# Performance work log

Measured on AMD Instinct MI355X. Metric: run time of the kernel, lower is better.

The kernel has to match this reference:

```python
import jax, jax.numpy as jnp
import numpy as np

EPS = 1e-5  # torch LayerNorm default

def ln(x, g, b):
    mu = jnp.mean(x, axis=-1, keepdims=True)
    var = jnp.mean((x - mu) ** 2, axis=-1, keepdims=True)
    return (x - mu) * jax.lax.rsqrt(var + EPS) * g + b

B, S, E, A = 131072, 199, 3, 32
D_IN = S + 1  # state_dim + 1 (time feature)

def setup_inputs() -> dict:
    key = jax.random.key(0)
    ks = iter(jax.random.split(key, 32))
    def w(shape, fan_in):
        lim = 1.0 / np.sqrt(fan_in)
        return jax.random.uniform(next(ks), shape, jnp.float32, -lim, lim)
    inp = {
        "state": jax.random.normal(next(ks), (B, S), jnp.float32),
        "time_delta": jax.random.uniform(next(ks), (B,), jnp.float32),
        # trunk: Linear(200,256)+LN, Linear(256,256)+LN, Linear(256,128)+LN
        "W1": w((D_IN, 256), D_IN), "b1": w((256,), D_IN),
        "g1": jnp.ones((256,), jnp.float32), "be1": jnp.zeros((256,), jnp.float32),
        "W2": w((256, 256), 256), "b2": w((256,), 256),
        "g2": jnp.ones((256,), jnp.float32), "be2": jnp.zeros((256,), jnp.float32),
        "W3": w((256, 128), 256), "b3": w((128,), 256),
        "g3": jnp.ones((128,), jnp.float32), "be3": jnp.zeros((128,), jnp.float32),
        # value stream
        "Wv1": w((128, 64), 128), "bv1": w((64,), 128),
        "gv": jnp.ones((64,), jnp.float32), "bev": jnp.zeros((64,), jnp.float32),
        "Wv2": w((64, 1), 64), "bv2": w((1,), 64),
        # E stacked advantage streams (all heads share action dim A)
        "Wa1": w((E, 128, 64), 128), "ba1": w((E, 64), 128),
        "ga": jnp.ones((E, 64), jnp.float32), "bea": jnp.zeros((E, 64), jnp.float32),
        "Wa2": w((E, 64, A), 64), "ba2": w((E, A), 64),
        "event_type": jax.random.randint(next(ks), (B,), 0, E),
    }
    return inp

def reference(state, time_delta,
              W1, b1, g1, be1, W2, b2, g2, be2, W3, b3, g3, be3,
              Wv1, bv1, gv, bev, Wv2, bv2,
              Wa1, ba1, ga, bea, Wa2, ba2, event_type):
    td = time_delta[:, None]                       # [B,1]
    x = jnp.concatenate([state, td], axis=1)       # [B,200]
    h = jax.nn.relu(ln(x @ W1 + b1, g1, be1))      # [B,256]
    h = jax.nn.relu(ln(h @ W2 + b2, g2, be2))      # [B,256]
    f = jax.nn.relu(ln(h @ W3 + b3, g3, be3))      # [B,128]
    v = jax.nn.relu(ln(f @ Wv1 + bv1, gv, bev)) @ Wv2 + bv2  # [B,1]
    # compute all E advantage heads, then per-sample select by event_type
    h1 = jnp.einsum('bd,edh->ebh', f, Wa1) + ba1[:, None, :]           # [E,B,64]
    h1 = jax.nn.relu(ln(h1, ga[:, None, :], bea[:, None, :]))
    adv_all = jnp.einsum('ebh,eha->eba', h1, Wa2) + ba2[:, None, :]    # [E,B,A]
    adv = jnp.take_along_axis(adv_all, event_type[None, :, None], axis=0)[0]  # [B,A]
    return v + (adv - adv.mean(axis=1, keepdims=True))
```

## Files before the change

kernel.cpp:

```cpp
#include <hip/hip_runtime.h>
#include <hip/hip_bf16.h>
#include <stdint.h>

#define DEV __device__ __forceinline__

typedef __attribute__((ext_vector_type(8))) short short8;
typedef __attribute__((ext_vector_type(4))) float floatx4;

constexpr int TM  = 64;
constexpr int NB  = 131072;
constexpr int AST = 264;

constexpr int OFF_W1 = 0;
constexpr int OFF_W2 = 57344;
constexpr int OFF_W3 = 122880;
constexpr int OFF_WH = 155648;
constexpr int OFF_WA2= 188416;
constexpr int NWQ    = 194560;

constexpr int C_B1=0, C_G1=256, C_BE1=512, C_B2=768, C_G2=1024, C_BE2=1280,
  C_B3=1536, C_G3=1664, C_BE3=1792, C_BV1=1920, C_GV=1984, C_BEV=2048,
  C_WV2=2112, C_BV2=2176, C_BA1=2180, C_GA=2372, C_BEA=2564, C_BA2=2756;
constexpr int NCONST=2852;

struct Ptrs {
  const float *state,*td,*W1,*b1,*g1,*be1,*W2,*b2,*g2,*be2,*W3,*b3,*g3,*be3,
    *Wv1,*bv1,*gv,*bev,*Wv2,*bv2,*Wa1,*ba1,*ga,*bea,*Wa2,*ba2;
  const int *et;
};

DEV unsigned short f2bf(float x){
  uint32_t u = __float_as_uint(x);
  u += 0x7fffu + ((u>>16)&1u);
  return (unsigned short)(u>>16);
}
DEV uint32_t f2bf_pk(float a, float b){
  float2 f2; f2.x=a; f2.y=b;
  __hip_bfloat162 h = __float22bfloat162_rn(f2);
  union { __hip_bfloat162 h; uint32_t u; } cv; cv.h = h;
  return cv.u;
}

__global__ void prep_kernel(Ptrs p, unsigned short* __restrict__ wq, float* __restrict__ cq){
  int idx = blockIdx.x*256 + threadIdx.x;
  if (idx < NWQ) {
    float v = 0.f;
    if (idx < OFF_W2) {
      int e = idx, w = e/14336, r = e%14336;
      int kc = r>>11, ct=(r>>9)&3, l=(r>>3)&63, j=r&7;
      int n = w*64 + ct*16 + (l&15);
      int k = kc*32 + (l>>4)*8 + j;
      if (k < 200) v = p.W1[k*256 + n];
      else if (k == 200) v = p.b1[n];
    } else if (idx < OFF_W3) {
      int e = idx-OFF_W2, w=e>>14, r=e&16383;
      int kc=r>>11, ct=(r>>9)&3, l=(r>>3)&63, j=r&7;
      int n = w*64 + ct*16 + (l&15);
      int k = kc*32 + (l>>4)*8 + j;
      v = p.W2[k*256 + n];
    } else if (idx < OFF_WH) {
      int e = idx-OFF_W3, w=e>>13, r=e&8191;
      int kc=r>>10, ct=(r>>9)&1, l=(r>>3)&63, j=r&7;
      int n = w*32 + ct*16 + (l&15);
      int k = kc*32 + (l>>4)*8 + j;
      v = p.W3[k*128 + n];
    } else if (idx < OFF_WA2) {
      int e = idx-OFF_WH, h=e>>13, r=e&8191;
      int kc=r>>11, ct=(r>>9)&3, l=(r>>3)&63, j=r&7;
      int n = ct*16 + (l&15);
      int k = kc*32 + (l>>4)*8 + j;
      v = (h<3) ? p.Wa1[h*8192 + k*64 + n] : p.Wv1[k*64 + n];
    } else {
      int e = idx-OFF_WA2, h=e>>11, r=e&2047;
      int kc=r>>10, ct=(r>>9)&1, l=(r>>3)&63, j=r&7;
      int n = ct*16 + (l&15);
      int k = kc*32 + (l>>4)*8 + j;
      v = p.Wa2[h*2048 + k*32 + n];
    }
    wq[idx] = f2bf(v);
  } else if (idx < NWQ + NCONST) {
    int ci = idx - NWQ;
    float v;
    if      (ci < 256)  v = p.b1[ci];
    else if (ci < 512)  v = p.g1[ci-256];
    else if (ci < 768)  v = p.be1[ci-512];
    else if (ci < 1024) v = p.b2[ci-768];
    else if (ci < 1280) v = p.g2[ci-1024];
    else if (ci < 1536) v = p.be2[ci-1280];
    else if (ci < 1664) v = p.b3[ci-1536];
    else if (ci < 1792) v = p.g3[ci-1664];
    else if (ci < 1920) v = p.be3[ci-1792];
    else if (ci < 1984) v = p.bv1[ci-1920];
    else if (ci < 2048) v = p.gv[ci-1984];
    else if (ci < 2112) v = p.bev[ci-2048];
    else if (ci < 2176) v = p.Wv2[ci-2112];
    else if (ci < 2180) v = (ci==2176) ? p.bv2[0] : 0.f;
    else if (ci < 2372) v = p.ba1[ci-2180];
    else if (ci < 2564) v = p.ga[ci-2372];
    else if (ci < 2756) v = p.bea[ci-2564];
    else                v = p.ba2[ci-2756];
    cq[ci] = v;
  }
}

template<int RT>
DEV void zeroAccT(floatx4 (&acc)[RT][4]){
  const floatx4 z = {0.f,0.f,0.f,0.f};
  #pragma unroll
  for (int rt=0;rt<RT;rt++)
    #pragma unroll
    for (int ct=0;ct<4;ct++) acc[rt][ct]=z;
}

template<int RT>
DEV void biasAccT(floatx4 (&acc)[RT][4], const float* __restrict__ cqb, int q){
  #pragma unroll
  for (int rt=0;rt<RT;rt++){
    floatx4 b4 = *(const floatx4*)(cqb + rt*16 + q*4);
    #pragma unroll
    for (int ct=0;ct<4;ct++) acc[rt][ct]=b4;
  }
}

template<int KC,int RT>
DEV void runGemmW(floatx4 (&acc)[RT][4], const unsigned short* __restrict__ wp,
                  const unsigned short* __restrict__ aB, int aOff, int lane){
  __builtin_amdgcn_s_setprio(1);
  #pragma unroll
  for (int kc=0;kc<KC;kc++){
    short8 a[4];
    #pragma unroll
    for (int c=0;c<4;c++)
      a[c] = *(const short8*)(aB + c*16*AST + aOff + kc*32);
    #pragma unroll
    for (int rt=0;rt<RT;rt++){
      short8 bw = *(const short8*)(wp + (kc*RT+rt)*512 + lane*8);
      #pragma unroll
      for (int c=0;c<4;c++)
        acc[rt][c] = __builtin_amdgcn_mfma_f32_16x16x32_bf16(bw, a[c], acc[rt][c], 0,0,0);
    }
  }
  __builtin_amdgcn_s_setprio(0);
}

template<int RT>
DEV void statsS(const floatx4 (&acc)[RT][4],
                float (&sst)[2][64][4], int w, int q, int ln){
  #pragma unroll
  for (int ct=0;ct<4;ct++){
    float s=0.f, ss=0.f;
    #pragma unroll
    for (int rt=0;rt<RT;rt++)
      #pragma unroll
      for (int r=0;r<4;r++){ float v=acc[rt][ct][r]; s+=v; ss+=v*v; }
    s += __shfl_xor(s,16); ss += __shfl_xor(ss,16);
    s += __shfl_xor(s,32); ss += __shfl_xor(ss,32);
    if (q==0){
      sst[0][ct*16+ln][w] = s;
      sst[1][ct*16+ln][w] = ss;
    }
  }
}

template<int RT>
DEV void lnWriteS(const floatx4 (&acc)[RT][4], const float* __restrict__ cq, int go, int beo,
                  const float (&sst)[2][64][4], float invN,
                  unsigned short* act_, int colBase, int q, int ln){
  float mu[4], rs[4];
  #pragma unroll
  for (int ct=0;ct<4;ct++){
    int row = ct*16+ln;
    floatx4 s4 = *(const floatx4*)&sst[0][row][0];
    floatx4 q4 = *(const floatx4*)&sst[1][row][0];
    float sv = (s4[0]+s4[1])+(s4[2]+s4[3]);
    float qv = (q4[0]+q4[1])+(q4[2]+q4[3]);
    mu[ct] = sv*invN;
    rs[ct] = rsqrtf(qv*invN - mu[ct]*mu[ct] + 1e-5f);
  }
  #pragma unroll
  for (int rt=0;rt<RT;rt++){
    floatx4 g4  = *(const floatx4*)(cq + go  + rt*16 + q*4);
    floatx4 be4 = *(const floatx4*)(cq + beo + rt*16 + q*4);
    #pragma unroll
    for (int ct=0;ct<4;ct++){
      float y[4];
      #pragma unroll
      for (int r=0;r<4;r++)
        y[r] = fmaxf((acc[rt][ct][r]-mu[ct])*rs[ct]*g4[r]+be4[r], 0.f);
      uint2 pk; pk.x = f2bf_pk(y[0],y[1]); pk.y = f2bf_pk(y[2],y[3]);
      *(uint2*)(act_ + (ct*16+ln)*AST + colBase + rt*16 + q*4) = pk;
    }
  }
}

__global__ __launch_bounds__(256,4) void dqn_main(
    const float* __restrict__ state, const float* __restrict__ td,
    const int* __restrict__ et, const unsigned short* __restrict__ wq,
    const float* __restrict__ cq, float* __restrict__ out)
{
  __shared__ __align__(16) unsigned short act[TM*AST];
  __shared__ __align__(16) float sstat[2][64][4];
  __shared__ float vbuf[64];
  __shared__ int   etl[64];

  const int tid=threadIdx.x, w=tid>>6, lane=tid&63, q=lane>>4, ln=lane&15;
  const int rowBlk = blockIdx.x*TM;

  const unsigned short* wl1 = wq + OFF_W1 + w*14336;
  const unsigned short* wl2 = wq + OFF_W2 + w*16384;
  const unsigned short* wl3 = wq + OFF_W3 + w*8192;
  const unsigned short* wlh = wq + OFF_WH + w*8192;
  const unsigned short* aBase = act + ln*AST + q*8;

  {
    const float* sbase = state + (size_t)rowBlk*199;
    #pragma unroll
    for (int it=0; it<7; ++it){
      int t = tid + it*256;
      int r = t/28, c = t - r*28;
      unsigned short* dst = act + r*AST + c*8;
      if (c < 25){
        const float* src = sbase + r*199 + c*8;
        float v0=src[0], v1=src[1], v2=src[2], v3=src[3];
        float v4=src[4], v5=src[5], v6=src[6];
        int o7 = (c==24)? 198 : c*8+7;
        float s7 = sbase[r*199 + o7];
        float v7 = (c==24)? td[rowBlk+r] : s7;
        uint4 pk;
        pk.x=f2bf_pk(v0,v1); pk.y=f2bf_pk(v2,v3);
        pk.z=f2bf_pk(v4,v5); pk.w=f2bf_pk(v6,v7);
        *(uint4*)dst = pk;
      } else {
        uint4 pk{0u,0u,0u,0u};
        if (c==25) pk.x = 0x3F80u;
        *(uint4*)dst = pk;
      }
    }
    if (tid < 64) etl[tid] = et[rowBlk+tid];
  }
  __syncthreads();

  floatx4 acc[4][4];

  zeroAccT<4>(acc);
  runGemmW<7,4>(acc, wl1, aBase, 0, lane);
  statsS<4>(acc, sstat, w, q, ln);
  __syncthreads();
  lnWriteS<4>(acc, cq, C_G1+w*64, C_BE1+w*64, sstat, 1.f/256.f, act, w*64, q, ln);
  __syncthreads();

  biasAccT<4>(acc, cq + C_B2 + w*64, q);
  runGemmW<8,4>(acc, wl2, aBase, 0, lane);
  statsS<4>(acc, sstat, w, q, ln);
  __syncthreads();
  lnWriteS<4>(acc, cq, C_G2+w*64, C_BE2+w*64, sstat, 1.f/256.f, act, w*64, q, ln);
  __syncthreads();

  floatx4 acc3[2][4];
  biasAccT<2>(acc3, cq + C_B3 + w*32, q);
  runGemmW<8,2>(acc3, wl3, aBase, 0, lane);
  statsS<2>(acc3, sstat, w, q, ln);
  __syncthreads();
  lnWriteS<2>(acc3, cq, C_G3+w*32, C_BE3+w*32, sstat, 1.f/128.f, act, w*32, q, ln);
  __syncthreads();

  const int bo = (w<3)? C_BA1+w*64 : C_BV1;
  const int go = (w<3)? C_GA +w*64 : C_GV;
  const int beo= (w<3)? C_BEA+w*64 : C_BEV;
  biasAccT<4>(acc, cq + bo, q);
  runGemmW<4,4>(acc, wlh, aBase, 0, lane);
  {
    float mu[4], rs[4];
    #pragma unroll
    for (int ct=0;ct<4;ct++){
      float s=0.f, ss=0.f;
      #pragma unroll
      for (int rt=0;rt<4;rt++)
        #pragma unroll
        for (int r=0;r<4;r++){ float v=acc[rt][ct][r]; s+=v; ss+=v*v; }
      s += __shfl_xor(s,16); ss += __shfl_xor(ss,16);
      s += __shfl_xor(s,32); ss += __shfl_xor(ss,32);
      mu[ct]=s*(1.f/64.f);
      rs[ct]=rsqrtf(ss*(1.f/64.f)-mu[ct]*mu[ct]+1e-5f);
    }
    #pragma unroll
    for (int rt=0;rt<4;rt++){
      floatx4 g4  = *(const floatx4*)(cq + go  + rt*16 + q*4);
      floatx4 be4 = *(const floatx4*)(cq + beo + rt*16 + q*4);
      #pragma unroll
      for (int ct=0;ct<4;ct++)
        #pragma unroll
        for (int r=0;r<4;r++)
          acc[rt][ct][r] = fmaxf((acc[rt][ct][r]-mu[ct])*rs[ct]*g4[r]+be4[r], 0.f);
    }
    if (w==3){
      float bv2v = cq[C_BV2];
      floatx4 wv4[4];
      #pragma unroll
      for (int rt=0;rt<4;rt++) wv4[rt] = *(const floatx4*)(cq + C_WV2 + rt*16 + q*4);
      #pragma unroll
      for (int ct=0;ct<4;ct++){
        float dot=0.f;
        #pragma unroll
        for (int rt=0;rt<4;rt++)
          #pragma unroll
          for (int r=0;r<4;r++) dot += acc[rt][ct][r]*wv4[rt][r];
        dot += __shfl_xor(dot,16);
        dot += __shfl_xor(dot,32);
        if (q==0) vbuf[ct*16+ln] = dot + bv2v;
      }
    }
  }
  __syncthreads();

  if (w<3){
    #pragma unroll
    for (int rt=0;rt<4;rt++)
      #pragma unroll
      for (int ct=0;ct<4;ct++){
        uint2 pk;
        pk.x = f2bf_pk(acc[rt][ct][0], acc[rt][ct][1]);
        pk.y = f2bf_pk(acc[rt][ct][2], acc[rt][ct][3]);
        *(uint2*)(act + (ct*16+ln)*AST + 64*w + rt*16 + q*4) = pk;
      }
    floatx4 acc2[2][4];
    biasAccT<2>(acc2, cq + C_BA2 + w*32, q);
    runGemmW<2,2>(acc2, wq + OFF_WA2 + w*2048, aBase, 64*w, lane);
    #pragma unroll
    for (int ct=0;ct<4;ct++){
      float sm=0.f;
      #pragma unroll
      for (int rt=0;rt<2;rt++)
        #pragma unroll
        for (int r=0;r<4;r++) sm += acc2[rt][ct][r];
      sm += __shfl_xor(sm,16);
      sm += __shfl_xor(sm,32);
      int b = ct*16+ln;
      if (etl[b]==w){
        float vm = vbuf[b] - sm*(1.f/32.f);
        #pragma unroll
        for (int rt=0;rt<2;rt++){
          floatx4 o = acc2[rt][ct];
          o[0]+=vm; o[1]+=vm; o[2]+=vm; o[3]+=vm;
          *(floatx4*)(out + (size_t)(rowBlk+b)*32 + rt*16 + q*4) = o;
        }
      }
    }
  }
}

extern "C" void kernel_launch(void* const* d_in, const int* in_sizes, int n_in,
                              void* d_out, int out_size, void* d_ws, size_t ws_size,
                              hipStream_t stream)
{
  Ptrs p;
  p.state=(const float*)d_in[0];  p.td =(const float*)d_in[1];
  p.W1 =(const float*)d_in[2];  p.b1 =(const float*)d_in[3];  p.g1 =(const float*)d_in[4];  p.be1=(const float*)d_in[5];
  p.W2 =(const float*)d_in[6];  p.b2 =(const float*)d_in[7];  p.g2 =(const float*)d_in[8];  p.be2=(const float*)d_in[9];
  p.W3 =(const float*)d_in[10]; p.b3 =(const float*)d_in[11]; p.g3 =(const float*)d_in[12]; p.be3=(const float*)d_in[13];
  p.Wv1=(const float*)d_in[14]; p.bv1=(const float*)d_in[15]; p.gv =(const float*)d_in[16]; p.bev=(const float*)d_in[17];
  p.Wv2=(const float*)d_in[18]; p.bv2=(const float*)d_in[19];
  p.Wa1=(const float*)d_in[20]; p.ba1=(const float*)d_in[21]; p.ga =(const float*)d_in[22]; p.bea=(const float*)d_in[23];
  p.Wa2=(const float*)d_in[24]; p.ba2=(const float*)d_in[25];
  p.et =(const int*)d_in[26];

  unsigned short* wq = (unsigned short*)d_ws;
  float* cq = (float*)((char*)d_ws + (size_t)NWQ*2);

  const int prepN = NWQ + NCONST;
  hipLaunchKernelGGL(prep_kernel, dim3((prepN+255)/256), dim3(256), 0, stream, p, wq, cq);
  hipLaunchKernelGGL(dqn_main, dim3(NB/TM), dim3(256), 0, stream,
                     p.state, p.td, p.et, (const unsigned short*)wq, (const float*)cq, (float*)d_out);
}
```

Baseline: 274.2 us.

## Double row tile to 128 with 512-thread blocks, two warps sharing each weight slice

Each block now processes 128 rows with 8 warps. Each pair of warps shares one weight column slice and splits the rows into two halves of 64. This is meant to amortize the per-block fixed costs and the weight streaming through cache over more rows. LDS per block roughly doubles, 512-thread blocks under launch_bounds(512,4) may limit occupancy or register budget, and each barrier now synchronizes more warps.

Measured after the change: 278.6 us. About the same (+1.6%).

```diff
diff --git a/kernel.cpp b/kernel.cpp
--- a/kernel.cpp
+++ b/kernel.cpp
@@ -7,7 +7,7 @@
 typedef __attribute__((ext_vector_type(8))) short short8;
 typedef __attribute__((ext_vector_type(4))) float floatx4;
 
-constexpr int TM  = 64;
+constexpr int TM  = 128;
 constexpr int NB  = 131072;
 constexpr int AST = 264;
 
@@ -145,7 +145,7 @@
 
 template<int RT>
 DEV void statsS(const floatx4 (&acc)[RT][4],
-                float (&sst)[2][64][4], int w, int q, int ln){
+                float (&sst)[2][TM][4], int ws, int rowOff, int q, int ln){
   #pragma unroll
   for (int ct=0;ct<4;ct++){
     float s=0.f, ss=0.f;
@@ -156,20 +156,20 @@
     s += __shfl_xor(s,16); ss += __shfl_xor(ss,16);
     s += __shfl_xor(s,32); ss += __shfl_xor(ss,32);
     if (q==0){
-      sst[0][ct*16+ln][w] = s;
-      sst[1][ct*16+ln][w] = ss;
+      sst[0][rowOff+ct*16+ln][ws] = s;
+      sst[1][rowOff+ct*16+ln][ws] = ss;
     }
   }
 }
 
 template<int RT>
 DEV void lnWriteS(const floatx4 (&acc)[RT][4], const float* __restrict__ cq, int go, int beo,
-                  const float (&sst)[2][64][4], float invN,
-                  unsigned short* act_, int colBase, int q, int ln){
+                  const float (&sst)[2][TM][4], float invN,
+                  unsigned short* act_, int colBase, int rowOff, int q, int ln){
   float mu[4], rs[4];
   #pragma unroll
   for (int ct=0;ct<4;ct++){
-    int row = ct*16+ln;
+    int row = rowOff + ct*16+ln;
     floatx4 s4 = *(const floatx4*)&sst[0][row][0];
     floatx4 q4 = *(const floatx4*)&sst[1][row][0];
     float sv = (s4[0]+s4[1])+(s4[2]+s4[3]);
@@ -188,35 +188,37 @@
       for (int r=0;r<4;r++)
         y[r] = fmaxf((acc[rt][ct][r]-mu[ct])*rs[ct]*g4[r]+be4[r], 0.f);
       uint2 pk; pk.x = f2bf_pk(y[0],y[1]); pk.y = f2bf_pk(y[2],y[3]);
-      *(uint2*)(act_ + (ct*16+ln)*AST + colBase + rt*16 + q*4) = pk;
-    }
-  }
-}
-
-__global__ __launch_bounds__(256,4) void dqn_main(
+      *(uint2*)(act_ + (rowOff+ct*16+ln)*AST + colBase + rt*16 + q*4) = pk;
+    }
+  }
+}
+
+__global__ __launch_bounds__(512,4) void dqn_main(
     const float* __restrict__ state, const float* __restrict__ td,
     const int* __restrict__ et, const unsigned short* __restrict__ wq,
     const float* __restrict__ cq, float* __restrict__ out)
 {
   __shared__ __align__(16) unsigned short act[TM*AST];
-  __shared__ __align__(16) float sstat[2][64][4];
-  __shared__ float vbuf[64];
-  __shared__ int   etl[64];
+  __shared__ __align__(16) float sstat[2][TM][4];
+  __shared__ float vbuf[TM];
+  __shared__ int   etl[TM];
 
   const int tid=threadIdx.x, w=tid>>6, lane=tid&63, q=lane>>4, ln=lane&15;
+  const int ws = w>>1, bh = w&1;
+  const int rowOff = bh*64;
   const int rowBlk = blockIdx.x*TM;
 
-  const unsigned short* wl1 = wq + OFF_W1 + w*14336;
-  const unsigned short* wl2 = wq + OFF_W2 + w*16384;
-  const unsigned short* wl3 = wq + OFF_W3 + w*8192;
-  const unsigned short* wlh = wq + OFF_WH + w*8192;
-  const unsigned short* aBase = act + ln*AST + q*8;
+  const unsigned short* wl1 = wq + OFF_W1 + ws*14336;
+  const unsigned short* wl2 = wq + OFF_W2 + ws*16384;
+  const unsigned short* wl3 = wq + OFF_W3 + ws*8192;
+  const unsigned short* wlh = wq + OFF_WH + ws*8192;
+  const unsigned short* aBase = act + (rowOff+ln)*AST + q*8;
 
   {
     const float* sbase = state + (size_t)rowBlk*199;
     #pragma unroll
     for (int it=0; it<7; ++it){
-      int t = tid + it*256;
+      int t = tid + it*512;
       int r = t/28, c = t - r*28;
       unsigned short* dst = act + r*AST + c*8;
       if (c < 25){
@@ -236,7 +238,7 @@
         *(uint4*)dst = pk;
       }
     }
-    if (tid < 64) etl[tid] = et[rowBlk+tid];
+    if (tid < TM) etl[tid] = et[rowBlk+tid];
   }
   __syncthreads();
 
@@ -244,29 +246,29 @@
 
   zeroAccT<4>(acc);
   runGemmW<7,4>(acc, wl1, aBase, 0, lane);
-  statsS<4>(acc, sstat, w, q, ln);
-  __syncthreads();
-  lnWriteS<4>(acc, cq, C_G1+w*64, C_BE1+w*64, sstat, 1.f/256.f, act, w*64, q, ln);
-  __syncthreads();
-
-  biasAccT<4>(acc, cq + C_B2 + w*64, q);
+  statsS<4>(acc, sstat, ws, rowOff, q, ln);
+  __syncthreads();
+  lnWriteS<4>(acc, cq, C_G1+ws*64, C_BE1+ws*64, sstat, 1.f/256.f, act, ws*64, rowOff, q, ln);
+  __syncthreads();
+
+  biasAccT<4>(acc, cq + C_B2 + ws*64, q);
   runGemmW<8,4>(acc, wl2, aBase, 0, lane);
-  statsS<4>(acc, sstat, w, q, ln);
-  __syncthreads();
-  lnWriteS<4>(acc, cq, C_G2+w*64, C_BE2+w*64, sstat, 1.f/256.f, act, w*64, q, ln);
+  statsS<4>(acc, sstat, ws, rowOff, q, ln);
+  __syncthreads();
+  lnWriteS<4>(acc, cq, C_G2+ws*64, C_BE2+ws*64, sstat, 1.f/256.f, act, ws*64, rowOff, q, ln);
   __syncthreads();
 
   floatx4 acc3[2][4];
-  biasAccT<2>(acc3, cq + C_B3 + w*32, q);
+  biasAccT<2>(acc3, cq + C_B3 + ws*32, q);
   runGemmW<8,2>(acc3, wl3, aBase, 0, lane);
-  statsS<2>(acc3, sstat, w, q, ln);
-  __syncthreads();
-  lnWriteS<2>(acc3, cq, C_G3+w*32, C_BE3+w*32, sstat, 1.f/128.f, act, w*32, q, ln);
-  __syncthreads();
-
-  const int bo = (w<3)? C_BA1+w*64 : C_BV1;
-  const int go = (w<3)? C_GA +w*64 : C_GV;
-  const int beo= (w<3)? C_BEA+w*64 : C_BEV;
+  statsS<2>(acc3, sstat, ws, rowOff, q, ln);
+  __syncthreads();
+  lnWriteS<2>(acc3, cq, C_G3+ws*32, C_BE3+ws*32, sstat, 1.f/128.f, act, ws*32, rowOff, q, ln);
+  __syncthreads();
+
+  const int bo = (ws<3)? C_BA1+ws*64 : C_BV1;
+  const int go = (ws<3)? C_GA +ws*64 : C_GV;
+  const int beo= (ws<3)? C_BEA+ws*64 : C_BEV;
   biasAccT<4>(acc, cq + bo, q);
   runGemmW<4,4>(acc, wlh, aBase, 0, lane);
   {
@@ -293,7 +295,7 @@
         for (int r=0;r<4;r++)
           acc[rt][ct][r] = fmaxf((acc[rt][ct][r]-mu[ct])*rs[ct]*g4[r]+be4[r], 0.f);
     }
-    if (w==3){
+    if (ws==3){
       float bv2v = cq[C_BV2];
       floatx4 wv4[4];
       #pragma unroll
@@ -307,13 +309,13 @@
           for (int r=0;r<4;r++) dot += acc[rt][ct][r]*wv4[rt][r];
         dot += __shfl_xor(dot,16);
         dot += __shfl_xor(dot,32);
-        if (q==0) vbuf[ct*16+ln] = dot + bv2v;
+        if (q==0) vbuf[rowOff + ct*16+ln] = dot + bv2v;
       }
     }
   }
   __syncthreads();
 
-  if (w<3){
+  if (ws<3){
     #pragma unroll
     for (int rt=0;rt<4;rt++)
       #pragma unroll
@@ -321,11 +323,11 @@
         uint2 pk;
         pk.x = f2bf_pk(acc[rt][ct][0], acc[rt][ct][1]);
         pk.y = f2bf_pk(acc[rt][ct][2], acc[rt][ct][3]);
-        *(uint2*)(act + (ct*16+ln)*AST + 64*w + rt*16 + q*4) = pk;
+        *(uint2*)(act + (rowOff+ct*16+ln)*AST + 64*ws + rt*16 + q*4) = pk;
       }
     floatx4 acc2[2][4];
-    biasAccT<2>(acc2, cq + C_BA2 + w*32, q);
-    runGemmW<2,2>(acc2, wq + OFF_WA2 + w*2048, aBase, 64*w, lane);
+    biasAccT<2>(acc2, cq + C_BA2 + ws*32, q);
+    runGemmW<2,2>(acc2, wq + OFF_WA2 + ws*2048, aBase, 64*ws, lane);
     #pragma unroll
     for (int ct=0;ct<4;ct++){
       float sm=0.f;
@@ -335,8 +337,8 @@
         for (int r=0;r<4;r++) sm += acc2[rt][ct][r];
       sm += __shfl_xor(sm,16);
       sm += __shfl_xor(sm,32);
-      int b = ct*16+ln;
-      if (etl[b]==w){
+      int b = rowOff + ct*16+ln;
+      if (etl[b]==ws){
         float vm = vbuf[b] - sm*(1.f/32.f);
         #pragma unroll
         for (int rt=0;rt<2;rt++){
@@ -369,6 +371,6 @@
 
   const int prepN = NWQ + NCONST;
   hipLaunchKernelGGL(prep_kernel, dim3((prepN+255)/256), dim3(256), 0, stream, p, wq, cq);
-  hipLaunchKernelGGL(dqn_main, dim3(NB/TM), dim3(256), 0, stream,
+  hipLaunchKernelGGL(dqn_main, dim3(NB/TM), dim3(512), 0, stream,
                      p.state, p.td, p.et, (const unsigned short*)wq, (const float*)cq, (float*)d_out);
 }
```
